# Performance work log

Hardware: AMD Instinct MI355X
Metric: run time of the kernel (lower is better)

## Reference

```python
import jax, jax.numpy as jnp
import numpy as np

EMBED = 1024
HEADS = 16
HEAD_DIM = EMBED // HEADS
MAX_REL = 8
B, S = 4, 1024


def setup_inputs() -> dict:
    key = jax.random.key(0)
    ks = jax.random.split(key, 12)
    lim = 1.0 / np.sqrt(EMBED)
    def lin(k):
        k1, k2 = jax.random.split(k)
        W = jax.random.uniform(k1, (EMBED, EMBED), jnp.float32, -lim, lim)
        b = jax.random.uniform(k2, (EMBED,), jnp.float32, -lim, lim)
        return W, b
    Wq, bq = lin(ks[0]); Wk, bk = lin(ks[1]); Wv, bv = lin(ks[2]); Wo, bo = lin(ks[3])
    return {
        'query': jax.random.normal(ks[4], (B, S, EMBED), jnp.float32),
        'key': jax.random.normal(ks[5], (B, S, EMBED), jnp.float32),
        'value': jax.random.normal(ks[6], (B, S, EMBED), jnp.float32),
        'mask': jnp.zeros((B, S, S), dtype=bool),
        'Wq': Wq, 'bq': bq, 'Wk': Wk, 'bk': bk, 'Wv': Wv, 'bv': bv,
        'Wo': Wo, 'bo': bo,
        'rel_bias': jnp.zeros((HEADS, 2 * MAX_REL + 1), jnp.float32),
    }


def _split_heads(x):
    b, s, _ = x.shape
    return x.reshape(b, s, HEADS, HEAD_DIM).transpose(0, 2, 1, 3)  # [b,h,s,d]


def reference(query, key, value, mask, Wq, bq, Wk, bk, Wv, bv, Wo, bo, rel_bias):
    scale = jnp.sqrt(jnp.float32(HEAD_DIM))
    Q = _split_heads(query @ Wq.T + bq)
    K = _split_heads(key @ Wk.T + bk)
    V = _split_heads(value @ Wv.T + bv)
    scores = jnp.einsum('bhqd,bhkd->bhqk', Q, K) / scale
    # relative position bias: rel_bias[h, clip(j-i)+max]
    idx = jnp.arange(query.shape[1])
    rel = jnp.clip(idx[None, :] - idx[:, None], -MAX_REL, MAX_REL) + MAX_REL  # [s,s]
    bias = rel_bias[:, rel]  # [h,s,s]
    scores = scores + bias[None]
    scores = jnp.where(mask[:, None, :, :], -jnp.inf, scores)
    attn = jax.nn.softmax(scores, axis=-1)
    ctx = jnp.einsum('bhqk,bhkd->bhqd', attn, V)
    b, h, s, d = ctx.shape
    out = ctx.transpose(0, 2, 1, 3).reshape(b, s, h * d) @ Wo.T + bo
    return out, attn, scores
```

## Files before the change

kernel.cpp:

```cpp
#include <hip/hip_runtime.h>

typedef __bf16 bf16_t;
typedef bf16_t bf16x4 __attribute__((ext_vector_type(4)));
typedef bf16_t bf16x8 __attribute__((ext_vector_type(8)));
typedef float f32x4 __attribute__((ext_vector_type(4)));
typedef float f32x8 __attribute__((ext_vector_type(8)));

#define B_N 4
#define S_N 1024
#define E_N 1024
#define H_N 16
#define D_N 64

#define MFMA16 __builtin_amdgcn_mfma_f32_16x16x32_bf16

static __device__ __forceinline__ bf16_t f2b(float x) { return (bf16_t)x; }

static __device__ __forceinline__ void gload_lds16(const void* g, void* l) {
  __builtin_amdgcn_global_load_lds(
      (const __attribute__((address_space(1))) unsigned int*)g,
      (__attribute__((address_space(3))) unsigned int*)l, 16, 0, 0);
}

static __device__ __forceinline__ void lds_barrier() {
  asm volatile("s_waitcnt lgkmcnt(0)\n\ts_barrier" ::: "memory");
  __builtin_amdgcn_sched_barrier(0);
}

__global__ __launch_bounds__(256) void convert_kernel(
    const float* __restrict__ q, const float* __restrict__ k, const float* __restrict__ v,
    const float* __restrict__ wq, const float* __restrict__ wk,
    const float* __restrict__ wv, const float* __restrict__ wo,
    bf16_t* __restrict__ dq, bf16_t* __restrict__ dk, bf16_t* __restrict__ dv,
    bf16_t* __restrict__ dwq, bf16_t* __restrict__ dwk,
    bf16_t* __restrict__ dwv, bf16_t* __restrict__ dwo)
{
  const size_t e = ((size_t)blockIdx.x * 256 + threadIdx.x) * 8;
  const float* src; bf16_t* dst; size_t off;
  if (e < 12582912ull) {
    const int which = (int)(e >> 22);
    off = e & 4194303ull;
    src = which == 0 ? q : (which == 1 ? k : v);
    dst = which == 0 ? dq : (which == 1 ? dk : dv);
  } else {
    const size_t e2 = e - 12582912ull;
    const int which = (int)(e2 >> 20);
    off = e2 & 1048575ull;
    src = which == 0 ? wq : (which == 1 ? wk : (which == 2 ? wv : wo));
    dst = which == 0 ? dwq : (which == 1 ? dwk : (which == 2 ? dwv : dwo));
  }
  f32x8 x = *(const f32x8*)(src + off);
  bf16x8 r;
#pragma unroll
  for (int i = 0; i < 8; ++i) r[i] = f2b(x[i]);
  *(bf16x8*)(dst + off) = r;
}

__global__ __launch_bounds__(256) void mask_rowany(
    const unsigned char* __restrict__ mask, unsigned char* __restrict__ flags)
{
  const int row = blockIdx.x * 4 + (threadIdx.x >> 6);
  const int lane = threadIdx.x & 63;
  const uint4 v = *(const uint4*)(mask + (size_t)row * 1024 + lane * 16);
  const unsigned int any = v.x | v.y | v.z | v.w;
  const unsigned long long bal = __ballot(any != 0);
  if (lane == 0) flags[row] = bal ? 1 : 0;
}

__global__ __launch_bounds__(256) void qkv_gemm(
    const bf16_t* __restrict__ qA, const bf16_t* __restrict__ kA, const bf16_t* __restrict__ vA,
    const bf16_t* __restrict__ Wq, const bf16_t* __restrict__ Wk, const bf16_t* __restrict__ Wv,
    const float* __restrict__ bq, const float* __restrict__ bk, const float* __restrict__ bv,
    bf16_t* __restrict__ Qo, bf16_t* __restrict__ Ko, bf16_t* __restrict__ Vto)
{
  const int z = blockIdx.z;
  const bf16_t* A = z == 0 ? qA : (z == 1 ? kA : vA);
  const bf16_t* W = z == 0 ? Wq : (z == 1 ? Wk : Wv);
  const float* bias = z == 0 ? bq : (z == 1 ? bk : bv);

  __shared__ bf16_t As[128 * 32];
  __shared__ bf16_t Bs[128 * 32];
  const int tid = threadIdx.x;
  const int m0 = blockIdx.y * 128, n0 = blockIdx.x * 128;
  const int lane = tid & 63, wid = tid >> 6;
  const int wr = wid >> 1, wc = wid & 1;
  const int lr = lane & 15, lh = lane >> 4;
  const int sr = lane >> 2, sc = (lane & 3) * 8;
  f32x4 acc[4][4] = {};
  for (int k0 = 0; k0 < 1024; k0 += 32) {
#pragma unroll
    for (int i = 0; i < 2; ++i) {
      const int br = wid * 32 + i * 16;
      gload_lds16(&A[(size_t)(m0 + br + sr) * 1024 + k0 + sc], &As[br * 32]);
      gload_lds16(&W[(size_t)(n0 + br + sr) * 1024 + k0 + sc], &Bs[br * 32]);
    }
    __syncthreads();
    bf16x8 af[4], bw[4];
#pragma unroll
    for (int m = 0; m < 4; ++m)
      af[m] = *(const bf16x8*)&As[(wr * 64 + m * 16 + lr) * 32 + lh * 8];
#pragma unroll
    for (int n = 0; n < 4; ++n)
      bw[n] = *(const bf16x8*)&Bs[(wc * 64 + n * 16 + lr) * 32 + lh * 8];
#pragma unroll
    for (int m = 0; m < 4; ++m)
#pragma unroll
      for (int n = 0; n < 4; ++n)
        acc[m][n] = MFMA16(af[m], bw[n], acc[m][n], 0, 0, 0);
    __syncthreads();
  }
#pragma unroll
  for (int n = 0; n < 4; ++n) {
    const int col = n0 + wc * 64 + n * 16 + lr;
    const float bv_ = bias[col];
    const int h = col >> 6, d = col & 63;
#pragma unroll
    for (int m = 0; m < 4; ++m) {
      const int row0 = m0 + wr * 64 + m * 16 + lh * 4;
#pragma unroll
      for (int r = 0; r < 4; ++r) {
        const int row = row0 + r;
        const float v = acc[m][n][r] + bv_;
        const int b = row >> 10, s = row & 1023;
        if (z == 0)
          Qo[((size_t)(b * H_N + h) * S_N + s) * D_N + d] = f2b(v);
        else if (z == 1)
          Ko[((size_t)(b * H_N + h) * S_N + s) * D_N + d] = f2b(v);
        else
          Vto[((size_t)(b * H_N + h) * D_N + d) * S_N + s] = f2b(v);
      }
    }
  }
}

__global__ __launch_bounds__(256) void out_gemm(
    const bf16_t* __restrict__ A, const bf16_t* __restrict__ W,
    const float* __restrict__ bias, float* __restrict__ Co)
{
  __shared__ bf16_t As[128 * 32];
  __shared__ bf16_t Bs[128 * 32];
  const int tid = threadIdx.x;
  const int m0 = blockIdx.y * 128, n0 = blockIdx.x * 128;
  const int lane = tid & 63, wid = tid >> 6;
  const int wr = wid >> 1, wc = wid & 1;
  const int lr = lane & 15, lh = lane >> 4;
  const int sr = lane >> 2, sc = (lane & 3) * 8;
  f32x4 acc[4][4] = {};
  for (int k0 = 0; k0 < 1024; k0 += 32) {
#pragma unroll
    for (int i = 0; i < 2; ++i) {
      const int br = wid * 32 + i * 16;
      gload_lds16(&A[(size_t)(m0 + br + sr) * 1024 + k0 + sc], &As[br * 32]);
      gload_lds16(&W[(size_t)(n0 + br + sr) * 1024 + k0 + sc], &Bs[br * 32]);
    }
    __syncthreads();
    bf16x8 af[4], bw[4];
#pragma unroll
    for (int m = 0; m < 4; ++m)
      af[m] = *(const bf16x8*)&As[(wr * 64 + m * 16 + lr) * 32 + lh * 8];
#pragma unroll
    for (int n = 0; n < 4; ++n)
      bw[n] = *(const bf16x8*)&Bs[(wc * 64 + n * 16 + lr) * 32 + lh * 8];
#pragma unroll
    for (int m = 0; m < 4; ++m)
#pragma unroll
      for (int n = 0; n < 4; ++n)
        acc[m][n] = MFMA16(af[m], bw[n], acc[m][n], 0, 0, 0);
    __syncthreads();
  }
#pragma unroll
  for (int n = 0; n < 4; ++n) {
    const int col = n0 + wc * 64 + n * 16 + lr;
    const float bv_ = bias[col];
#pragma unroll
    for (int m = 0; m < 4; ++m) {
      const int row0 = m0 + wr * 64 + m * 16 + lh * 4;
#pragma unroll
      for (int r = 0; r < 4; ++r)
        Co[(size_t)(row0 + r) * E_N + col] = acc[m][n][r] + bv_;
    }
  }
}

static __device__ __forceinline__ f32x4 score4(
    f32x4 acc, int qrow, int kc, const unsigned char* __restrict__ mrow,
    const float* __restrict__ rbh, float rb_lo, float rb_hi, bool um)
{
  const int d0 = kc - qrow;
  float b0, b1, b2, b3;
  if (d0 >= 8) { b0 = b1 = b2 = b3 = rb_hi; }
  else if (d0 <= -11) { b0 = b1 = b2 = b3 = rb_lo; }
  else {
    int dd;
    dd = d0;     dd = dd < -8 ? -8 : (dd > 8 ? 8 : dd); b0 = rbh[dd + 8];
    dd = d0 + 1; dd = dd < -8 ? -8 : (dd > 8 ? 8 : dd); b1 = rbh[dd + 8];
    dd = d0 + 2; dd = dd < -8 ? -8 : (dd > 8 ? 8 : dd); b2 = rbh[dd + 8];
    dd = d0 + 3; dd = dd < -8 ? -8 : (dd > 8 ? 8 : dd); b3 = rbh[dd + 8];
  }
  f32x4 s;
  s[0] = acc[0] * 0.125f + b0;
  s[1] = acc[1] * 0.125f + b1;
  s[2] = acc[2] * 0.125f + b2;
  s[3] = acc[3] * 0.125f + b3;
  if (um) {
    const unsigned int mw = *(const unsigned int*)(mrow + kc);
    const float NEG = -__builtin_inff();
    if (mw & 0xffu)       s[0] = NEG;
    if (mw & 0xff00u)     s[1] = NEG;
    if (mw & 0xff0000u)   s[2] = NEG;
    if (mw & 0xff000000u) s[3] = NEG;
  }
  return s;
}

__global__ __launch_bounds__(256) void fused_attn(
    const bf16_t* __restrict__ Q, const bf16_t* __restrict__ K,
    const bf16_t* __restrict__ Vt,
    const unsigned char* __restrict__ mask, const unsigned char* __restrict__ rowflag,
    const float* __restrict__ rel_bias,
    float* __restrict__ scores, float* __restrict__ attn, bf16_t* __restrict__ ctx)
{
  __shared__ bf16_t Ktile[64 * 64];
  __shared__ bf16_t Vtile[64 * 64];
  __shared__ float S_lds[4][16][68];

  const int bh = blockIdx.y, b = bh >> 4, h = bh & 15;
  const int q0 = blockIdx.x * 64;
  const int tid = threadIdx.x;
  const int w = tid >> 6, lane = tid & 63;
  const int lr = lane & 15, lh = lane >> 4;
  const int qrow = q0 + w * 16 + lr;

  const bf16_t* Qh = Q + (size_t)bh * (S_N * D_N);
  const bf16_t* Kh = K + (size_t)bh * (S_N * D_N);
  const bf16_t* Vh = Vt + (size_t)bh * (D_N * S_N);
  const unsigned char* mrow = mask + (size_t)b * S_N * S_N + (size_t)qrow * S_N;
  float* Sbase = scores + (size_t)bh * S_N * S_N + (size_t)(q0 + w * 16) * S_N;
  float* Abase = attn + (size_t)bh * S_N * S_N + (size_t)(q0 + w * 16) * S_N;
  const float* rbh = rel_bias + h * 17;
  const float rb_lo = rbh[0], rb_hi = rbh[16];
  const float NEG = -__builtin_inff();
  const float THR = 8.0f;
  const bool um = rowflag[b * S_N + qrow] != 0;

  const int sg_row0 = tid >> 3, sg_c = tid & 7;
  const int sg_row1 = (tid + 256) >> 3;
  const int sg_s0 = (sg_c ^ (sg_row0 & 7)) * 8;
  const int sg_s1 = (sg_c ^ (sg_row1 & 7)) * 8;

  bf16x8 qa0 = *(const bf16x8*)&Qh[(size_t)qrow * D_N + lh * 8];
  bf16x8 qa1 = *(const bf16x8*)&Qh[(size_t)qrow * D_N + 32 + lh * 8];

  const int ks0 = (lh ^ (lr & 7)) * 8;
  const int ks1 = ((4 + lh) ^ (lr & 7)) * 8;

  float mrun = NEG, srun = 0.f;
  for (int kt = 0; kt < 16; ++kt) {
    const int kb = kt * 64;
    lds_barrier();
    *(bf16x8*)&Ktile[sg_row0 * 64 + sg_s0] =
        *(const bf16x8*)&Kh[(size_t)(kb + sg_row0) * D_N + sg_c * 8];
    *(bf16x8*)&Ktile[sg_row1 * 64 + sg_s1] =
        *(const bf16x8*)&Kh[(size_t)(kb + sg_row1) * D_N + sg_c * 8];
    lds_barrier();
    f32x4 sr4[4];
    float mloc = NEG;
#pragma unroll
    for (int t = 0; t < 4; ++t) {
      const int krow = t * 16 + lr;
      bf16x8 ka0 = *(const bf16x8*)&Ktile[krow * 64 + ks0];
      bf16x8 ka1 = *(const bf16x8*)&Ktile[krow * 64 + ks1];
      f32x4 acc = {};
      acc = MFMA16(ka0, qa0, acc, 0, 0, 0);
      acc = MFMA16(ka1, qa1, acc, 0, 0, 0);
      const int kc = kb + t * 16 + 4 * lh;
      f32x4 s = score4(acc, qrow, kc, mrow, rbh, rb_lo, rb_hi, um);
      sr4[t] = s;
      *(f32x4*)&S_lds[w][lr][t * 16 + 4 * lh] = s;
      mloc = fmaxf(mloc, fmaxf(fmaxf(s[0], s[1]), fmaxf(s[2], s[3])));
    }
    mloc = fmaxf(mloc, __shfl_xor(mloc, 16));
    mloc = fmaxf(mloc, __shfl_xor(mloc, 32));
    if (__any(mloc - mrun > THR)) {
      const float mn = fmaxf(mrun, mloc);
      if (mn > NEG) {
        srun = srun * __expf(mrun - mn);
        mrun = mn;
      }
    }
    const bool live = mrun > NEG;
    float ls = 0.f;
#pragma unroll
    for (int t = 0; t < 4; ++t) {
      f32x4 s = sr4[t];
      float e0 = live ? __expf(s[0] - mrun) : 0.f;
      float e1 = live ? __expf(s[1] - mrun) : 0.f;
      float e2 = live ? __expf(s[2] - mrun) : 0.f;
      float e3 = live ? __expf(s[3] - mrun) : 0.f;
      ls += (e0 + e1) + (e2 + e3);
    }
    srun += ls;
#pragma unroll
    for (int i = 0; i < 4; ++i) {
      const int row = 4 * i + lh;
      f32x4 sv = *(const f32x4*)&S_lds[w][row][lr * 4];
      __builtin_nontemporal_store(sv, (f32x4*)&Sbase[(size_t)row * S_N + kb + lr * 4]);
    }
  }
  srun += __shfl_xor(srun, 16);
  srun += __shfl_xor(srun, 32);
  const float M = mrun;
  const float invs = 1.0f / srun;

  f32x4 accp[4] = {};
  for (int kt = 0; kt < 16; ++kt) {
    const int kb = kt * 64;
    lds_barrier();
    *(bf16x8*)&Ktile[sg_row0 * 64 + sg_s0] =
        *(const bf16x8*)&Kh[(size_t)(kb + sg_row0) * D_N + sg_c * 8];
    *(bf16x8*)&Ktile[sg_row1 * 64 + sg_s1] =
        *(const bf16x8*)&Kh[(size_t)(kb + sg_row1) * D_N + sg_c * 8];
    *(bf16x8*)&Vtile[sg_row0 * 64 + sg_s0] =
        *(const bf16x8*)&Vh[(size_t)sg_row0 * S_N + kb + sg_c * 8];
    *(bf16x8*)&Vtile[sg_row1 * 64 + sg_s1] =
        *(const bf16x8*)&Vh[(size_t)sg_row1 * S_N + kb + sg_c * 8];
    lds_barrier();
#pragma unroll
    for (int t = 0; t < 4; ++t) {
      const int krow = t * 16 + lr;
      bf16x8 ka0 = *(const bf16x8*)&Ktile[krow * 64 + ks0];
      bf16x8 ka1 = *(const bf16x8*)&Ktile[krow * 64 + ks1];
      f32x4 acc = {};
      acc = MFMA16(ka0, qa0, acc, 0, 0, 0);
      acc = MFMA16(ka1, qa1, acc, 0, 0, 0);
      const int kc = kb + t * 16 + 4 * lh;
      f32x4 s = score4(acc, qrow, kc, mrow, rbh, rb_lo, rb_hi, um);
      f32x4 p;
#pragma unroll
      for (int j = 0; j < 4; ++j) p[j] = __expf(s[j] - M) * invs;
      *(f32x4*)&S_lds[w][lr][t * 16 + 4 * lh] = p;
    }
#pragma unroll
    for (int i = 0; i < 4; ++i) {
      const int row = 4 * i + lh;
      f32x4 pv = *(const f32x4*)&S_lds[w][row][lr * 4];
      __builtin_nontemporal_store(pv, (f32x4*)&Abase[(size_t)row * S_N + kb + lr * 4]);
    }
#pragma unroll
    for (int ch = 0; ch < 2; ++ch) {
      f32x8 pf = *(const f32x8*)&S_lds[w][lr][ch * 32 + lh * 8];
      bf16x8 pa;
#pragma unroll
      for (int j = 0; j < 8; ++j) pa[j] = f2b(pf[j]);
#pragma unroll
      for (int dt = 0; dt < 4; ++dt) {
        const int drow = dt * 16 + lr;
        bf16x8 vb = *(const bf16x8*)&Vtile[drow * 64 + (((ch * 4 + lh) ^ (lr & 7)) * 8)];
        accp[dt] = MFMA16(pa, vb, accp[dt], 0, 0, 0);
      }
    }
  }
#pragma unroll
  for (int dt = 0; dt < 4; ++dt)
#pragma unroll
    for (int r = 0; r < 4; ++r)
      ctx[((size_t)(b * S_N + q0 + w * 16 + 4 * lh + r)) * E_N + h * 64 + dt * 16 + lr] =
          f2b(accp[dt][r]);
}

extern "C" void kernel_launch(void* const* d_in, const int* in_sizes, int n_in,
                              void* d_out, int out_size, void* d_ws, size_t ws_size,
                              hipStream_t stream) {
  (void)in_sizes; (void)n_in; (void)out_size; (void)ws_size;
  const float* query = (const float*)d_in[0];
  const float* key   = (const float*)d_in[1];
  const float* value = (const float*)d_in[2];
  const unsigned char* mask = (const unsigned char*)d_in[3];
  const float* Wq = (const float*)d_in[4];
  const float* bq = (const float*)d_in[5];
  const float* Wk = (const float*)d_in[6];
  const float* bk = (const float*)d_in[7];
  const float* Wv = (const float*)d_in[8];
  const float* bv = (const float*)d_in[9];
  const float* Wo = (const float*)d_in[10];
  const float* bo = (const float*)d_in[11];
  const float* rel_bias = (const float*)d_in[12];

  float* out_f    = (float*)d_out;
  float* attn_f   = out_f + (size_t)4194304;
  float* scores_f = attn_f + (size_t)67108864;

  char* ws = (char*)d_ws;
  bf16_t* qbf  = (bf16_t*)(ws);
  bf16_t* kbf  = (bf16_t*)(ws + (8ull  << 20));
  bf16_t* vbf  = (bf16_t*)(ws + (16ull << 20));
  bf16_t* Wqb  = (bf16_t*)(ws + (24ull << 20));
  bf16_t* Wkb  = (bf16_t*)(ws + (26ull << 20));
  bf16_t* Wvb  = (bf16_t*)(ws + (28ull << 20));
  bf16_t* Wob  = (bf16_t*)(ws + (30ull << 20));
  bf16_t* Qbf  = (bf16_t*)(ws + (32ull << 20));
  bf16_t* Kbf  = (bf16_t*)(ws + (40ull << 20));
  bf16_t* Vtbf = (bf16_t*)(ws + (48ull << 20));
  bf16_t* CTX  = (bf16_t*)(ws + (56ull << 20));
  unsigned char* FLAGS = (unsigned char*)(ws + (64ull << 20));

  convert_kernel<<<dim3(8192), dim3(256), 0, stream>>>(
      query, key, value, Wq, Wk, Wv, Wo, qbf, kbf, vbf, Wqb, Wkb, Wvb, Wob);
  mask_rowany<<<dim3(1024), dim3(256), 0, stream>>>(mask, FLAGS);
  qkv_gemm<<<dim3(8, 32, 3), dim3(256), 0, stream>>>(
      qbf, kbf, vbf, Wqb, Wkb, Wvb, bq, bk, bv, Qbf, Kbf, Vtbf);
  fused_attn<<<dim3(16, 64), dim3(256), 0, stream>>>(
      Qbf, Kbf, Vtbf, mask, FLAGS, rel_bias, scores_f, attn_f, CTX);
  out_gemm<<<dim3(8, 32), dim3(256), 0, stream>>>(CTX, Wob, bo, out_f);
}
```

Measured before the change: 223.0 us.

## Use 512-thread attention blocks with 128 queries and remapped block order

The fused attention kernel now runs 8 waves per block covering 128 query rows, so each K/V tile staged in LDS is shared by twice as many queries. Each thread loads a single 16-byte chunk per tile instead of two. Blocks are launched as a flat index and permuted so consecutive blocks spread across heads, which changes how K/V reuse lands in L2. This halves the grid to 512 blocks and doubles LDS for the score staging buffer, which may lower occupancy and load balance across CUs.

```diff
diff --git a/kernel.cpp b/kernel.cpp
--- a/kernel.cpp
+++ b/kernel.cpp
@@ -213,7 +213,7 @@
   return s;
 }
 
-__global__ __launch_bounds__(256) void fused_attn(
+__global__ __launch_bounds__(512) void fused_attn(
     const bf16_t* __restrict__ Q, const bf16_t* __restrict__ K,
     const bf16_t* __restrict__ Vt,
     const unsigned char* __restrict__ mask, const unsigned char* __restrict__ rowflag,
@@ -222,10 +222,14 @@
 {
   __shared__ bf16_t Ktile[64 * 64];
   __shared__ bf16_t Vtile[64 * 64];
-  __shared__ float S_lds[4][16][68];
-
-  const int bh = blockIdx.y, b = bh >> 4, h = bh & 15;
-  const int q0 = blockIdx.x * 64;
+  __shared__ float S_lds[8][16][68];
+
+  int flat = blockIdx.y * 4 + blockIdx.x;
+  flat = blockIdx.y * 4 + blockIdx.x;
+  flat = (flat & 7) * 64 + (flat >> 3);
+  const int bh = flat >> 3, b = bh >> 4, h = bh & 15;
+  const int q0 = (flat & 7) * 128;
+
   const int tid = threadIdx.x;
   const int w = tid >> 6, lane = tid & 63;
   const int lr = lane & 15, lh = lane >> 4;
@@ -243,10 +247,8 @@
   const float THR = 8.0f;
   const bool um = rowflag[b * S_N + qrow] != 0;
 
-  const int sg_row0 = tid >> 3, sg_c = tid & 7;
-  const int sg_row1 = (tid + 256) >> 3;
-  const int sg_s0 = (sg_c ^ (sg_row0 & 7)) * 8;
-  const int sg_s1 = (sg_c ^ (sg_row1 & 7)) * 8;
+  const int sg_row = tid >> 3, sg_c = tid & 7;
+  const int sg_s = (sg_c ^ (sg_row & 7)) * 8;
 
   bf16x8 qa0 = *(const bf16x8*)&Qh[(size_t)qrow * D_N + lh * 8];
   bf16x8 qa1 = *(const bf16x8*)&Qh[(size_t)qrow * D_N + 32 + lh * 8];
@@ -258,10 +260,8 @@
   for (int kt = 0; kt < 16; ++kt) {
     const int kb = kt * 64;
     lds_barrier();
-    *(bf16x8*)&Ktile[sg_row0 * 64 + sg_s0] =
-        *(const bf16x8*)&Kh[(size_t)(kb + sg_row0) * D_N + sg_c * 8];
-    *(bf16x8*)&Ktile[sg_row1 * 64 + sg_s1] =
-        *(const bf16x8*)&Kh[(size_t)(kb + sg_row1) * D_N + sg_c * 8];
+    *(bf16x8*)&Ktile[sg_row * 64 + sg_s] =
+        *(const bf16x8*)&Kh[(size_t)(kb + sg_row) * D_N + sg_c * 8];
     lds_barrier();
     f32x4 sr4[4];
     float mloc = NEG;
@@ -316,14 +316,10 @@
   for (int kt = 0; kt < 16; ++kt) {
     const int kb = kt * 64;
     lds_barrier();
-    *(bf16x8*)&Ktile[sg_row0 * 64 + sg_s0] =
-        *(const bf16x8*)&Kh[(size_t)(kb + sg_row0) * D_N + sg_c * 8];
-    *(bf16x8*)&Ktile[sg_row1 * 64 + sg_s1] =
-        *(const bf16x8*)&Kh[(size_t)(kb + sg_row1) * D_N + sg_c * 8];
-    *(bf16x8*)&Vtile[sg_row0 * 64 + sg_s0] =
-        *(const bf16x8*)&Vh[(size_t)sg_row0 * S_N + kb + sg_c * 8];
-    *(bf16x8*)&Vtile[sg_row1 * 64 + sg_s1] =
-        *(const bf16x8*)&Vh[(size_t)sg_row1 * S_N + kb + sg_c * 8];
+    *(bf16x8*)&Ktile[sg_row * 64 + sg_s] =
+        *(const bf16x8*)&Kh[(size_t)(kb + sg_row) * D_N + sg_c * 8];
+    *(bf16x8*)&Vtile[sg_row * 64 + sg_s] =
+        *(const bf16x8*)&Vh[(size_t)sg_row * S_N + kb + sg_c * 8];
     lds_barrier();
 #pragma unroll
     for (int t = 0; t < 4; ++t) {
@@ -409,7 +405,7 @@
   mask_rowany<<<dim3(1024), dim3(256), 0, stream>>>(mask, FLAGS);
   qkv_gemm<<<dim3(8, 32, 3), dim3(256), 0, stream>>>(
       qbf, kbf, vbf, Wqb, Wkb, Wvb, bq, bk, bv, Qbf, Kbf, Vtbf);
-  fused_attn<<<dim3(16, 64), dim3(256), 0, stream>>>(
+  fused_attn<<<dim3(4, 128), dim3(512), 0, stream>>>(
       Qbf, Kbf, Vtbf, mask, FLAGS, rel_bias, scores_f, attn_f, CTX);
   out_gemm<<<dim3(8, 32), dim3(256), 0, stream>>>(CTX, Wob, bo, out_f);
 }
```

Measured after the change: 216.4 us. 3.0% less time.
